# Optimization experiments

Hardware: AMD Instinct MI355X
Metric: run time of the kernel (lower is better)

## Reference

```python
import jax, jax.numpy as jnp
import numpy as np

INPUT_DIM, OUTPUT_DIM = 128, 256
FPS_FACTOR, KNN = 14, 10


def fps(pcd, K):
    """Farthest point sampling. pcd: [B,N,3] -> (points [B,K,3], indices [B,K]).
    Deterministic start at index 0 (pytorch3d uses first/random point)."""
    B, N, _ = pcd.shape
    first = jnp.zeros((B,), jnp.int32)
    init_d = jnp.full((B, N), 1e10, pcd.dtype)

    def step(carry, _):
        dists, last = carry
        lp = jnp.take_along_axis(pcd, last[:, None, None], axis=1)  # [B,1,3]
        d = jnp.sum((pcd - lp) ** 2, axis=-1)                        # [B,N]
        dists = jnp.minimum(dists, d)
        nxt = jnp.argmax(dists, axis=-1).astype(jnp.int32)
        return (dists, nxt), nxt

    (_, _), rest = jax.lax.scan(step, (init_d, first), None, length=K - 1)
    idx = jnp.concatenate([first[None, :], rest], axis=0).T  # [B,K]
    pts = jnp.take_along_axis(pcd, idx[..., None], axis=1)   # [B,K,3]
    return pts, idx


def knn_idx(q, p, k):
    """q:[B,Q,3], p:[B,N,3] -> nearest-neighbor indices [B,Q,k] (squared L2)."""
    d = (jnp.sum(q * q, -1)[:, :, None] + jnp.sum(p * p, -1)[:, None, :]
         - 2.0 * jnp.einsum('bqc,bnc->bqn', q, p))
    _, idx = jax.lax.top_k(-d, k)
    return idx


_bgather = jax.vmap(lambda a, i: a[i])  # per-batch fancy gather


def setup_inputs() -> dict:
    key = jax.random.key(0)
    k1, k2, k3, k4, k5 = jax.random.split(key, 5)
    B, N = 4, 16384
    tgt = jax.random.normal(k1, (B, N, INPUT_DIM), jnp.float32)
    pcd_x = jax.random.normal(k2, (B, N, 3), jnp.float32)
    pcd_v = jax.random.normal(k3, (B, N, 3, 3), jnp.float32)
    W = jax.random.normal(k4, (INPUT_DIM, OUTPUT_DIM), jnp.float32) / np.sqrt(INPUT_DIM)
    b = jax.random.normal(k5, (OUTPUT_DIM,), jnp.float32) * 0.01
    return {"tgt": tgt, "pcd_x": pcd_x, "pcd_v": pcd_v, "W": W, "b": b}


def reference(tgt, pcd_x, pcd_v, W, b):
    B, N, D = tgt.shape
    n_out = N // FPS_FACTOR
    out_pcd_x, out_indices = fps(pcd_x, n_out)          # [B,n_out,3], [B,n_out]
    nn = knn_idx(out_pcd_x, pcd_x, KNN)                 # [B,n_out,k]

    knn_pcd = _bgather(pcd_x, nn)                       # [B,n_out,k,3]
    query_f = jnp.take_along_axis(tgt, out_indices[..., None], axis=1)  # [B,n_out,D]
    query_c = out_pcd_x
    query_v = _bgather(pcd_v, out_indices)              # [B,n_out,V,3]
    key_f = _bgather(tgt, nn)                           # [B,n_out,k,D]
    key_c = knn_pcd
    key_v = _bgather(pcd_v, nn)                         # [B,n_out,k,V,3]

    # flatten (B*n_out) super-point groups, project features
    _query_f = query_f.reshape(-1, D)[:, None, :] @ W + b          # [B*n_out,1,O]
    _key_f = key_f.reshape(-1, KNN, D) @ W + b                     # [B*n_out,k,O]
    del _key_f, key_c, key_v  # consumed by the (identity stand-in) transformer

    # NOTE: URSATransformer stand-in = identity on the projected query features
    out_query_f = _query_f.reshape(B, n_out, OUTPUT_DIM)
    return out_query_f, query_c, query_v
```

## Files before the change

### kernel.cpp

```cpp
#include <hip/hip_runtime.h>

constexpr int B_   = 4;
constexpr int N_   = 16384;
constexpr int NOUT = 1170;
constexpr int D_   = 128;
constexpr int O_   = 256;

typedef float f32x2 __attribute__((ext_vector_type(2)));

constexpr int TPB_FPS = 512;
constexpr int PPT   = N_ / TPB_FPS;
constexpr int NPAIR = PPT / 2;
constexpr int NW    = TPB_FPS / 64;

__global__ __launch_bounds__(TPB_FPS, 2)
void fps_kernel(const float* __restrict__ pcd_x,
                int* __restrict__ sel,
                float* __restrict__ out_c) {
  const int b = blockIdx.x;
  const int t = threadIdx.x;
  const float* __restrict__ P = pcd_x + (size_t)b * N_ * 3;

  f32x2 x[NPAIR], y[NPAIR], z[NPAIR], dm[NPAIR];
#pragma unroll
  for (int k = 0; k < NPAIR; ++k) {
    const int p0 = t + (2 * k) * TPB_FPS;
    const int p1 = t + (2 * k + 1) * TPB_FPS;
    x[k]  = f32x2{P[p0 * 3 + 0], P[p1 * 3 + 0]};
    y[k]  = f32x2{P[p0 * 3 + 1], P[p1 * 3 + 1]};
    z[k]  = f32x2{P[p0 * 3 + 2], P[p1 * 3 + 2]};
    dm[k] = f32x2{1e10f, 1e10f};
  }

  __shared__ unsigned long long s_key[2][NW];

  float lx = P[0], ly = P[1], lz = P[2];
  if (t == 0) {
    sel[b * NOUT + 0] = 0;
    out_c[((size_t)b * NOUT + 0) * 3 + 0] = lx;
    out_c[((size_t)b * NOUT + 0) * 3 + 1] = ly;
    out_c[((size_t)b * NOUT + 0) * 3 + 2] = lz;
  }

  for (int step = 1; step < NOUT; ++step) {
    const f32x2 lxx = {lx, lx}, lyy = {ly, ly}, lzz = {lz, lz};
    f32x2 bv2 = {-1.0f, -1.0f};
    {
#pragma clang fp contract(off)
#pragma unroll
      for (int k = 0; k < NPAIR; ++k) {
        const f32x2 dx = x[k] - lxx;
        const f32x2 dy = y[k] - lyy;
        const f32x2 dz = z[k] - lzz;
        const f32x2 s  = (dx * dx + dy * dy) + dz * dz;
        f32x2 nd;
        nd.x = fminf(dm[k].x, s.x);
        nd.y = fminf(dm[k].y, s.y);
        dm[k] = nd;
        bv2.x = fmaxf(bv2.x, nd.x);
        bv2.y = fmaxf(bv2.y, nd.y);
      }
    }
    const float bv = fmaxf(bv2.x, bv2.y);

    int bi = 0;
#pragma unroll
    for (int k = NPAIR - 1; k >= 0; --k) {
      if (dm[k].y == bv) bi = t + (2 * k + 1) * TPB_FPS;
      if (dm[k].x == bv) bi = t + (2 * k) * TPB_FPS;
    }

    unsigned long long key =
        ((unsigned long long)__float_as_uint(bv) << 32) | (unsigned int)(~bi);

#pragma unroll
    for (int off = 32; off > 0; off >>= 1) {
      const unsigned long long ok = __shfl_xor(key, off, 64);
      if (ok > key) key = ok;
    }
    if ((t & 63) == 0) s_key[step & 1][t >> 6] = key;
    __syncthreads();

    unsigned long long kmax = s_key[step & 1][0];
#pragma unroll
    for (int w = 1; w < NW; ++w) {
      const unsigned long long kw = s_key[step & 1][w];
      if (kw > kmax) kmax = kw;
    }
    int ri = ~(unsigned int)kmax;
    ri = __builtin_amdgcn_readfirstlane(ri);

    lx = P[ri * 3 + 0];
    ly = P[ri * 3 + 1];
    lz = P[ri * 3 + 2];
    if (t == 0) {
      sel[b * NOUT + step] = ri;
      out_c[((size_t)b * NOUT + step) * 3 + 0] = lx;
      out_c[((size_t)b * NOUT + step) * 3 + 1] = ly;
      out_c[((size_t)b * NOUT + step) * 3 + 2] = lz;
    }
  }
}

constexpr int TPB_PROJ = 256;
constexpr int RPB = 4;

__global__ __launch_bounds__(TPB_PROJ)
void proj_kernel(const float* __restrict__ tgt,
                 const float* __restrict__ pcd_v,
                 const float* __restrict__ W,
                 const float* __restrict__ bias,
                 const int* __restrict__ sel,
                 float* __restrict__ out_f,
                 float* __restrict__ out_v) {
  const int t = threadIdx.x;
  const int row0 = blockIdx.x * RPB;

  __shared__ float sA[RPB * D_];
  __shared__ int   sIdx[RPB];

  if (t < RPB) {
    const int row = row0 + t;
    const int b = row / NOUT;
    sIdx[t] = b * N_ + sel[row];
  }
  __syncthreads();

#pragma unroll
  for (int l = 0; l < RPB * D_ / TPB_PROJ; ++l) {
    const int e = t + l * TPB_PROJ;
    const int r = e >> 7;
    const int k = e & (D_ - 1);
    sA[e] = tgt[(size_t)sIdx[r] * D_ + k];
  }
  __syncthreads();

  float acc0 = 0.f, acc1 = 0.f, acc2 = 0.f, acc3 = 0.f;
#pragma unroll 8
  for (int k = 0; k < D_; ++k) {
    const float w = W[k * O_ + t];
    acc0 = fmaf(sA[0 * D_ + k], w, acc0);
    acc1 = fmaf(sA[1 * D_ + k], w, acc1);
    acc2 = fmaf(sA[2 * D_ + k], w, acc2);
    acc3 = fmaf(sA[3 * D_ + k], w, acc3);
  }
  const float bb = bias[t];
  out_f[(size_t)(row0 + 0) * O_ + t] = acc0 + bb;
  out_f[(size_t)(row0 + 1) * O_ + t] = acc1 + bb;
  out_f[(size_t)(row0 + 2) * O_ + t] = acc2 + bb;
  out_f[(size_t)(row0 + 3) * O_ + t] = acc3 + bb;

  if (t < RPB * 9) {
    const int r = t / 9;
    const int e = t - r * 9;
    out_v[(size_t)(row0 + r) * 9 + e] = pcd_v[(size_t)sIdx[r] * 9 + e];
  }
}

extern "C" void kernel_launch(void* const* d_in, const int* in_sizes, int n_in,
                              void* d_out, int out_size, void* d_ws, size_t ws_size,
                              hipStream_t stream) {
  const float* tgt   = (const float*)d_in[0];
  const float* pcd_x = (const float*)d_in[1];
  const float* pcd_v = (const float*)d_in[2];
  const float* W     = (const float*)d_in[3];
  const float* bias  = (const float*)d_in[4];

  float* out   = (float*)d_out;
  float* out_f = out;
  float* out_c = out + (size_t)B_ * NOUT * O_;
  float* out_v = out_c + (size_t)B_ * NOUT * 3;

  int* sel = (int*)d_ws;

  hipLaunchKernelGGL(fps_kernel, dim3(B_), dim3(TPB_FPS), 0, stream,
                     pcd_x, sel, out_c);
  hipLaunchKernelGGL(proj_kernel, dim3(B_ * NOUT / RPB), dim3(TPB_PROJ), 0, stream,
                     tgt, pcd_v, W, bias, sel, out_f, out_v);
}
```

Baseline: 2.031 ms.

## Use 1024-thread FPS with DPP float max reduction and contiguous point ownership

Doubles the FPS block to 1024 threads so each thread holds half as many points. Each thread now owns a contiguous run of points, which keeps index tie-breaking consistent with a lowest-index rule. The per-wave 64-bit shuffle argmax is replaced by a DPP float max, a ballot, and a readlane to fetch the winning index. The 16 wave keys are then reduced with vectorised LDS reads. This aims to shorten the serial per-step reduction latency, at the cost of more waves joining each barrier and a single block per batch.

```diff
diff --git a/kernel.cpp b/kernel.cpp
--- a/kernel.cpp
+++ b/kernel.cpp
@@ -7,32 +7,47 @@
 constexpr int O_   = 256;
 
 typedef float f32x2 __attribute__((ext_vector_type(2)));
-
-constexpr int TPB_FPS = 512;
+typedef unsigned long long u64;
+
+template <int CTRL>
+__device__ __forceinline__ float dpp_fmax(float x) {
+  int yi = __builtin_amdgcn_update_dpp(__float_as_int(x), __float_as_int(x),
+                                       CTRL, 0xF, 0xF, false);
+  return fmaxf(x, __int_as_float(yi));
+}
+
+__device__ __forceinline__ u64 umax64(u64 a, u64 b) { return a > b ? a : b; }
+
+constexpr int TPB_FPS = 1024;
 constexpr int PPT   = N_ / TPB_FPS;
 constexpr int NPAIR = PPT / 2;
 constexpr int NW    = TPB_FPS / 64;
 
-__global__ __launch_bounds__(TPB_FPS, 2)
+__global__ __launch_bounds__(TPB_FPS)
+__attribute__((amdgpu_waves_per_eu(4, 4)))
 void fps_kernel(const float* __restrict__ pcd_x,
                 int* __restrict__ sel,
                 float* __restrict__ out_c) {
   const int b = blockIdx.x;
   const int t = threadIdx.x;
   const float* __restrict__ P = pcd_x + (size_t)b * N_ * 3;
+  const int base = t * PPT;
 
   f32x2 x[NPAIR], y[NPAIR], z[NPAIR], dm[NPAIR];
 #pragma unroll
   for (int k = 0; k < NPAIR; ++k) {
-    const int p0 = t + (2 * k) * TPB_FPS;
-    const int p1 = t + (2 * k + 1) * TPB_FPS;
-    x[k]  = f32x2{P[p0 * 3 + 0], P[p1 * 3 + 0]};
-    y[k]  = f32x2{P[p0 * 3 + 1], P[p1 * 3 + 1]};
-    z[k]  = f32x2{P[p0 * 3 + 2], P[p1 * 3 + 2]};
+    const int p0 = base + 2 * k;
+    x[k]  = f32x2{P[p0 * 3 + 0], P[p0 * 3 + 3]};
+    y[k]  = f32x2{P[p0 * 3 + 1], P[p0 * 3 + 4]};
+    z[k]  = f32x2{P[p0 * 3 + 2], P[p0 * 3 + 5]};
     dm[k] = f32x2{1e10f, 1e10f};
   }
-
-  __shared__ unsigned long long s_key[2][NW];
+#pragma unroll
+  for (int k = 0; k < NPAIR; ++k) {
+    asm volatile("" : "+v"(x[k]), "+v"(y[k]), "+v"(z[k]), "+v"(dm[k]));
+  }
+
+  __shared__ u64 s_key[2][NW] __attribute__((aligned(16)));
 
   float lx = P[0], ly = P[1], lz = P[2];
   if (t == 0) {
@@ -43,6 +58,7 @@
   }
 
   for (int step = 1; step < NOUT; ++step) {
+    const int par = step & 1;
     const f32x2 lxx = {lx, lx}, lyy = {ly, ly}, lzz = {lz, lz};
     f32x2 bv2 = {-1.0f, -1.0f};
     {
@@ -63,31 +79,45 @@
     }
     const float bv = fmaxf(bv2.x, bv2.y);
 
+    float wm = bv;
+    wm = dpp_fmax<0xB1>(wm);
+    wm = dpp_fmax<0x4E>(wm);
+    wm = dpp_fmax<0x141>(wm);
+    wm = dpp_fmax<0x140>(wm);
+    wm = dpp_fmax<0x142>(wm);
+    wm = dpp_fmax<0x143>(wm);
+    const float wmax =
+        __int_as_float(__builtin_amdgcn_readlane(__float_as_int(wm), 63));
+
     int bi = 0;
 #pragma unroll
     for (int k = NPAIR - 1; k >= 0; --k) {
-      if (dm[k].y == bv) bi = t + (2 * k + 1) * TPB_FPS;
-      if (dm[k].x == bv) bi = t + (2 * k) * TPB_FPS;
-    }
-
-    unsigned long long key =
-        ((unsigned long long)__float_as_uint(bv) << 32) | (unsigned int)(~bi);
-
-#pragma unroll
-    for (int off = 32; off > 0; off >>= 1) {
-      const unsigned long long ok = __shfl_xor(key, off, 64);
-      if (ok > key) key = ok;
-    }
-    if ((t & 63) == 0) s_key[step & 1][t >> 6] = key;
+      if (dm[k].y == bv) bi = base + 2 * k + 1;
+      if (dm[k].x == bv) bi = base + 2 * k;
+    }
+
+    const unsigned long long mask = __ballot(bv == wmax);
+    const int flane = __builtin_ctzll(mask);
+    const int idx_w = __builtin_amdgcn_readlane(bi, flane);
+
+    const u64 key =
+        ((u64)__float_as_uint(wmax) << 32) | (unsigned)(~idx_w);
+    if ((t & 63) == 0) s_key[par][t >> 6] = key;
     __syncthreads();
 
-    unsigned long long kmax = s_key[step & 1][0];
-#pragma unroll
-    for (int w = 1; w < NW; ++w) {
-      const unsigned long long kw = s_key[step & 1][w];
-      if (kw > kmax) kmax = kw;
-    }
-    int ri = ~(unsigned int)kmax;
+    const ulonglong2* kp =
+        reinterpret_cast<const ulonglong2*>(&s_key[par][0]);
+    u64 m[8];
+#pragma unroll
+    for (int i = 0; i < 8; ++i) {
+      const ulonglong2 v = kp[i];
+      m[i] = umax64(v.x, v.y);
+    }
+    const u64 q0 = umax64(umax64(m[0], m[1]), umax64(m[2], m[3]));
+    const u64 q1 = umax64(umax64(m[4], m[5]), umax64(m[6], m[7]));
+    const u64 kmax = umax64(q0, q1);
+
+    int ri = (int)(~(unsigned)kmax);
     ri = __builtin_amdgcn_readfirstlane(ri);
 
     lx = P[ri * 3 + 0];
```

Result: faster. 1.904 ms (-6.2%).
